# Optimization experiments

Hardware: AMD Instinct MI355X
Metric: run time of the kernel (lower is better)

The kernel has to match this reference:

```python
import jax, jax.numpy as jnp
import numpy as np

N, E, F, H, C, G = 100000, 1600000, 128, 4, 32, 64
D = H * C  # 128, per-layer node dim
NEG_SLOPE = 0.2
BN_EPS = 1e-5


def setup_inputs() -> dict:
    key = jax.random.key(0)
    ks = jax.random.split(key, 24)
    inp = {
        "x": jax.random.normal(ks[0], (N, F), jnp.float32),
        "edge_index": jax.random.randint(ks[1], (2, E), 0, N, jnp.int64),
        "batch": jnp.sort(jax.random.randint(ks[2], (N,), 0, G, jnp.int64)),
        # GATConv layer 0: in=F, out=C per head
        "w0": jax.random.normal(ks[3], (F, H * C), jnp.float32) * 0.1,
        "att_src0": jax.random.normal(ks[4], (H, C), jnp.float32) * 0.1,
        "att_dst0": jax.random.normal(ks[5], (H, C), jnp.float32) * 0.1,
        "bias0": jax.random.normal(ks[6], (H * C,), jnp.float32) * 0.1,
        # GATConv layer 1: in=D, out=C per head
        "w1": jax.random.normal(ks[7], (D, H * C), jnp.float32) * 0.1,
        "att_src1": jax.random.normal(ks[8], (H, C), jnp.float32) * 0.1,
        "att_dst1": jax.random.normal(ks[9], (H, C), jnp.float32) * 0.1,
        "bias1": jax.random.normal(ks[10], (H * C,), jnp.float32) * 0.1,
        # BatchNorm (eval mode: running stats)
        "bn_g0": jax.random.normal(ks[11], (D,), jnp.float32) * 0.1 + 1.0,
        "bn_b0": jax.random.normal(ks[12], (D,), jnp.float32) * 0.1,
        "bn_m0": jax.random.normal(ks[13], (D,), jnp.float32) * 0.1,
        "bn_v0": jax.random.uniform(ks[14], (D,), jnp.float32) + 0.5,
        "bn_g1": jax.random.normal(ks[15], (D,), jnp.float32) * 0.1 + 1.0,
        "bn_b1": jax.random.normal(ks[16], (D,), jnp.float32) * 0.1,
        "bn_m1": jax.random.normal(ks[17], (D,), jnp.float32) * 0.1,
        "bn_v1": jax.random.uniform(ks[18], (D,), jnp.float32) + 0.5,
        # head MLP
        "lin1_w": jax.random.normal(ks[19], (D, D // 2), jnp.float32) * 0.1,
        "lin1_b": jax.random.normal(ks[20], (D // 2,), jnp.float32) * 0.1,
        "lin2_w": jax.random.normal(ks[21], (D // 2, 1), jnp.float32) * 0.1,
        "lin2_b": jax.random.normal(ks[22], (1,), jnp.float32) * 0.1,
    }
    return inp


def gat_conv(x, src, dst, w, att_s, att_d, bias):
    """PyG GATConv (concat=True, add_self_loops already in src/dst), eval mode."""
    n = x.shape[0]
    h = (x @ w).reshape(n, H, C)                       # [N,H,C]
    a_s = jnp.sum(h * att_s, axis=-1)                   # [N,H]
    a_d = jnp.sum(h * att_d, axis=-1)                   # [N,H]
    e = jax.nn.leaky_relu(a_s[src] + a_d[dst], NEG_SLOPE)  # [Etot,H]
    m = jax.ops.segment_max(e, dst, num_segments=n)
    m = jax.lax.stop_gradient(jnp.where(jnp.isfinite(m), m, 0.0))
    ex = jnp.exp(e - m[dst])
    denom = jax.ops.segment_sum(ex, dst, num_segments=n)
    alpha = ex / (denom[dst] + 1e-16)                    # segment softmax over dst
    out = jax.ops.segment_sum(h[src] * alpha[:, :, None], dst, num_segments=n)
    return out.reshape(n, H * C) + bias


def bn_eval(x, g, b, m, v):
    return (x - m) * jax.lax.rsqrt(v + BN_EPS) * g + b


def reference(x, edge_index, batch,
              w0, att_src0, att_dst0, bias0,
              w1, att_src1, att_dst1, bias1,
              bn_g0, bn_b0, bn_m0, bn_v0,
              bn_g1, bn_b1, bn_m1, bn_v1,
              lin1_w, lin1_b, lin2_w, lin2_b):
    n = x.shape[0]
    loops = jnp.arange(n, dtype=edge_index.dtype)
    src = jnp.concatenate([edge_index[0], loops])
    dst = jnp.concatenate([edge_index[1], loops])

    h = gat_conv(x, src, dst, w0, att_src0, att_dst0, bias0)
    h = jax.nn.relu(bn_eval(h, bn_g0, bn_b0, bn_m0, bn_v0))
    h = gat_conv(h, src, dst, w1, att_src1, att_dst1, bias1)
    h = jax.nn.relu(bn_eval(h, bn_g1, bn_b1, bn_m1, bn_v1))

    # global mean pool over graphs
    summed = jax.ops.segment_sum(h, batch, num_segments=G)           # [G,D]
    counts = jax.ops.segment_sum(jnp.ones((n,), h.dtype), batch, num_segments=G)
    pooled = summed / jnp.maximum(counts, 1.0)[:, None]

    z = jax.nn.relu(pooled @ lin1_w + lin1_b)
    return z @ lin2_w + lin2_b                                        # [G,1]
```

## Files before the change

### kernel.cpp

```cpp
#include <hip/hip_runtime.h>

#define GG 64
#define STRIDE 10240
#define NBINMAX 256

typedef __attribute__((ext_vector_type(8))) short short8;
typedef __attribute__((ext_vector_type(4))) float f32x4;


__device__ inline unsigned short bf16rne(float f) {
  unsigned int x = __float_as_uint(f);
  unsigned int r = (x + 0x7FFFu + ((x >> 16) & 1u)) >> 16;
  return (unsigned short)r;
}
__device__ inline unsigned int pack2(float a, float b) {
  return (unsigned int)bf16rne(a) | ((unsigned int)bf16rne(b) << 16);
}
__device__ inline float blo(unsigned int v) { return __uint_as_float(v << 16); }
__device__ inline float bhi(unsigned int v) { return __uint_as_float(v & 0xFFFF0000u); }


__global__ __launch_bounds__(256) void part_p1(const int* __restrict__ ei,
                                               int* __restrict__ gcur,
                                               unsigned int* __restrict__ pairs,
                                               int E, int N) {
  __shared__ int hist[NBINMAX];
  __shared__ int gbase[NBINMAX];
  __shared__ int lcur[NBINMAX];
  int t = threadIdx.x;
  int tot = E + N;
  int base = blockIdx.x * 4096;
  hist[t] = 0;
  __syncthreads();
  int sarr[16], darr[16];
  #pragma unroll
  for (int k = 0; k < 16; ++k) {
    int i = base + k * 256 + t;
    if (i < tot) {
      int s, d;
      if (i < E) { s = ei[i]; d = ei[E + i]; } else { s = i - E; d = s; }
      sarr[k] = s; darr[k] = d;
      atomicAdd(&hist[d >> 9], 1);
    } else darr[k] = -1;
  }
  __syncthreads();
  int c = hist[t];
  gbase[t] = (c > 0) ? atomicAdd(&gcur[t], c) : 0;
  lcur[t] = 0;
  __syncthreads();
  #pragma unroll
  for (int k = 0; k < 16; ++k) {
    int d = darr[k];
    if (d >= 0) {
      int b = d >> 9;
      int p = gbase[b] + atomicAdd(&lcur[b], 1);
      pairs[p] = ((unsigned int)(d & 511) << 17) | (unsigned int)sarr[k];
    }
  }
}


__global__ __launch_bounds__(256) void part_p2(const unsigned int* __restrict__ pairs,
                                               const int* __restrict__ gcur,
                                               int* __restrict__ ssrc,
                                               int* __restrict__ offsets,
                                               int* __restrict__ counts, int N) {
  __shared__ int ncnt[512], ncur[512], excl_s[512];
  __shared__ int wsum[4];
  int b = blockIdx.x;
  int t = threadIdx.x;
  int pb = b * STRIDE;
  int cnt = gcur[b] - pb;
  ncnt[t] = 0; ncnt[t + 256] = 0;
  __syncthreads();
  for (int e = t; e < cnt; e += 256) {
    unsigned int v = pairs[pb + e];
    atomicAdd(&ncnt[v >> 17], 1);
  }
  __syncthreads();
  int c0 = ncnt[2 * t], c1 = ncnt[2 * t + 1];
  int ps = c0 + c1;
  int lane = t & 63, w = t >> 6;
  int x = ps;
  #pragma unroll
  for (int s = 1; s < 64; s <<= 1) { int y = __shfl_up(x, s); if (lane >= s) x += y; }
  if (lane == 63) wsum[w] = x;
  __syncthreads();
  int woff = 0;
  for (int i = 0; i < w; ++i) woff += wsum[i];
  int ep = woff + x - ps;
  excl_s[2 * t]     = ep;
  excl_s[2 * t + 1] = ep + c0;
  __syncthreads();
  int binstart = b << 9;
  for (int i = t; i < 512; i += 256) {
    ncur[i] = excl_s[i];
    int node = binstart + i;
    if (node < N) { offsets[node] = pb + excl_s[i]; counts[node] = ncnt[i]; }
  }
  __syncthreads();
  for (int e = t; e < cnt; e += 256) {
    unsigned int v = pairs[pb + e];
    int dl = v >> 17;
    int p = atomicAdd(&ncur[dl], 1);
    ssrc[pb + p] = (int)(v & 0x1FFFF);
  }
}


__global__ __launch_bounds__(256) void gbounds(const int* __restrict__ batch,
                                               int* __restrict__ gstart, int N) {
  int i = blockIdx.x * 256 + threadIdx.x;
  if (i >= N) return;
  int g = batch[i];
  if (i == 0 || batch[i - 1] != g) gstart[g] = i;
}

__global__ __launch_bounds__(64) void gfix(const int* __restrict__ gstart,
                                           int* __restrict__ go,
                                           int* __restrict__ ge, int N) {
  int g = threadIdx.x;
  int s = gstart[g];
  int v = (s < 0) ? 0x7FFFFFFF : s;
  int suf = v;
  #pragma unroll
  for (int off = 1; off < 64; off <<= 1) {
    int x = __shfl_down(suf, off);
    if (g + off < 64) suf = min(suf, x);
  }
  int nxt = __shfl_down(suf, 1);
  if (g == 63) nxt = 0x7FFFFFFF;
  int e = nxt == 0x7FFFFFFF ? N : nxt;
  if (s < 0) { go[g] = e; ge[g] = e; }
  else       { go[g] = s; ge[g] = e; }
}


__global__ __launch_bounds__(256) void wprep(const float* __restrict__ w0,
                                             const float* __restrict__ w1,
                                             unsigned short* __restrict__ wt,
                                             int* __restrict__ gcur) {
  if (blockIdx.x == 0) gcur[threadIdx.x] = threadIdx.x * STRIDE;
  int idx = blockIdx.x * 256 + threadIdx.x;
  int layer = idx >> 14;
  int e = idx & 16383;
  int k = e >> 7, n = e & 127;
  float v = (layer ? w1 : w0)[e];
  unsigned short hi = bf16rne(v);
  float hif = __uint_as_float((unsigned int)hi << 16);
  unsigned short lo = bf16rne(v - hif);
  unsigned short* basep = wt + layer * 32768;
  basep[n * 128 + k] = hi;
  basep[16384 + n * 128 + k] = lo;
}


template <int BF16IN>
__global__ __launch_bounds__(512) void gemm_mfma(
    const void* __restrict__ in_, const unsigned short* __restrict__ wtL,
    const float* __restrict__ att_s, const float* __restrict__ att_d,
    unsigned int* __restrict__ h16, float* __restrict__ a_s,
    float* __restrict__ a_d, int N) {
  __shared__ unsigned short xh[128][40];
  __shared__ unsigned short xl[BF16IN ? 1 : 128][40];
  int t = threadIdx.x;
  int base = blockIdx.x * 128;
  int lane = t & 63, w = t >> 6;
  int l15 = lane & 15, lg = lane >> 4;
  int hd = w & 3;
  int n0 = hd * 32;
  int rh = w >> 2;

  f32x4 zero4 = {0.f, 0.f, 0.f, 0.f};
  f32x4 acc[4][2];
  #pragma unroll
  for (int rt = 0; rt < 4; ++rt) { acc[rt][0] = zero4; acc[rt][1] = zero4; }

  int sr = t >> 2;
  int sc = (t & 3) * 8;
  int gr = base + sr;
  int rc = gr < N ? gr : (N - 1);
  const float* xpf = (const float*)in_ + (size_t)rc * 128 + sc;
  const unsigned int* xpb = (const unsigned int*)in_ + (size_t)rc * 64 + (sc >> 1);

  const unsigned short* wh0 = &wtL[(size_t)(n0 + l15) * 128];
  const unsigned short* wh1 = &wtL[(size_t)(n0 + 16 + l15) * 128];

  float4 u0, u1;
  uint4 p0;
  if constexpr (!BF16IN) {
    u0 = *(const float4*)(xpf + 0);
    u1 = *(const float4*)(xpf + 4);
  } else {
    p0 = *(const uint4*)(xpb + 0);
  }
  short8 cbh0 = *(const short8*)(wh0 + lg * 8);
  short8 cbh1 = *(const short8*)(wh1 + lg * 8);
  short8 cbl0 = *(const short8*)(wh0 + 16384 + lg * 8);
  short8 cbl1 = *(const short8*)(wh1 + 16384 + lg * 8);

  #pragma unroll
  for (int kt = 0; kt < 4; ++kt) {
    if (kt) __syncthreads();
    if constexpr (!BF16IN) {
      unsigned int b0 = __float_as_uint(u0.x), b1 = __float_as_uint(u0.y);
      unsigned int b2 = __float_as_uint(u0.z), b3 = __float_as_uint(u0.w);
      unsigned int b4 = __float_as_uint(u1.x), b5 = __float_as_uint(u1.y);
      unsigned int b6 = __float_as_uint(u1.z), b7 = __float_as_uint(u1.w);
      *(unsigned int*)&xh[sr][sc + 0] = __builtin_amdgcn_perm(b1, b0, 0x07060302u);
      *(unsigned int*)&xh[sr][sc + 2] = __builtin_amdgcn_perm(b3, b2, 0x07060302u);
      *(unsigned int*)&xh[sr][sc + 4] = __builtin_amdgcn_perm(b5, b4, 0x07060302u);
      *(unsigned int*)&xh[sr][sc + 6] = __builtin_amdgcn_perm(b7, b6, 0x07060302u);
      float r0 = u0.x - __uint_as_float(b0 & 0xFFFF0000u);
      float r1 = u0.y - __uint_as_float(b1 & 0xFFFF0000u);
      float r2 = u0.z - __uint_as_float(b2 & 0xFFFF0000u);
      float r3 = u0.w - __uint_as_float(b3 & 0xFFFF0000u);
      float r4 = u1.x - __uint_as_float(b4 & 0xFFFF0000u);
      float r5 = u1.y - __uint_as_float(b5 & 0xFFFF0000u);
      float r6 = u1.z - __uint_as_float(b6 & 0xFFFF0000u);
      float r7 = u1.w - __uint_as_float(b7 & 0xFFFF0000u);
      *(unsigned int*)&xl[sr][sc + 0] =
          __builtin_amdgcn_perm(__float_as_uint(r1), __float_as_uint(r0), 0x07060302u);
      *(unsigned int*)&xl[sr][sc + 2] =
          __builtin_amdgcn_perm(__float_as_uint(r3), __float_as_uint(r2), 0x07060302u);
      *(unsigned int*)&xl[sr][sc + 4] =
          __builtin_amdgcn_perm(__float_as_uint(r5), __float_as_uint(r4), 0x07060302u);
      *(unsigned int*)&xl[sr][sc + 6] =
          __builtin_amdgcn_perm(__float_as_uint(r7), __float_as_uint(r6), 0x07060302u);
    } else {
      *(uint4*)&xh[sr][sc] = p0;
    }
    __syncthreads();
    float4 v0 = u0, v1 = u1;
    uint4 q0 = p0;
    short8 nbh0 = cbh0, nbh1 = cbh1, nbl0 = cbl0, nbl1 = cbl1;
    if (kt < 3) {
      int k1 = (kt + 1) * 32;
      if constexpr (!BF16IN) {
        v0 = *(const float4*)(xpf + k1);
        v1 = *(const float4*)(xpf + k1 + 4);
      } else {
        q0 = *(const uint4*)(xpb + (k1 >> 1));
      }
      nbh0 = *(const short8*)(wh0 + k1 + lg * 8);
      nbh1 = *(const short8*)(wh1 + k1 + lg * 8);
      nbl0 = *(const short8*)(wh0 + 16384 + k1 + lg * 8);
      nbl1 = *(const short8*)(wh1 + 16384 + k1 + lg * 8);
    }
    #pragma unroll
    for (int rt = 0; rt < 4; ++rt) {
      int row = rh * 64 + rt * 16 + l15;
      short8 fah = *(const short8*)&xh[row][lg * 8];
      acc[rt][0] = __builtin_amdgcn_mfma_f32_16x16x32_bf16(fah, cbh0, acc[rt][0], 0, 0, 0);
      acc[rt][1] = __builtin_amdgcn_mfma_f32_16x16x32_bf16(fah, cbh1, acc[rt][1], 0, 0, 0);
      if constexpr (!BF16IN) {
        short8 fal = *(const short8*)&xl[row][lg * 8];
        acc[rt][0] = __builtin_amdgcn_mfma_f32_16x16x32_bf16(fal, cbh0, acc[rt][0], 0, 0, 0);
        acc[rt][1] = __builtin_amdgcn_mfma_f32_16x16x32_bf16(fal, cbh1, acc[rt][1], 0, 0, 0);
      }
      acc[rt][0] = __builtin_amdgcn_mfma_f32_16x16x32_bf16(fah, cbl0, acc[rt][0], 0, 0, 0);
      acc[rt][1] = __builtin_amdgcn_mfma_f32_16x16x32_bf16(fah, cbl1, acc[rt][1], 0, 0, 0);
    }
    u0 = v0; u1 = v1; p0 = q0;
    cbh0 = nbh0; cbh1 = nbh1; cbl0 = nbl0; cbl1 = nbl1;
  }

  int headg = hd;
  float as0 = att_s[n0 + l15], as1 = att_s[n0 + 16 + l15];
  float ad0 = att_d[n0 + l15], ad1 = att_d[n0 + 16 + l15];
  #pragma unroll
  for (int rt = 0; rt < 4; ++rt) {
    float ps[4], pd[4];
    #pragma unroll
    for (int q = 0; q < 4; ++q) {
      float c0v = acc[rt][0][q], c1v = acc[rt][1][q];
      float pp0 = __shfl_xor(c0v, 1), pp1 = __shfl_xor(c1v, 1);
      int row = base + rh * 64 + rt * 16 + lg * 4 + q;
      if (!(l15 & 1) && row < N) {
        h16[(size_t)row * 64 + (n0 + l15) / 2]      = pack2(c0v, pp0);
        h16[(size_t)row * 64 + (n0 + 16 + l15) / 2] = pack2(c1v, pp1);
      }
      ps[q] = c0v * as0 + c1v * as1;
      pd[q] = c0v * ad0 + c1v * ad1;
    }
    #pragma unroll
    for (int m = 1; m <= 8; m <<= 1) {
      #pragma unroll
      for (int q = 0; q < 4; ++q) { ps[q] += __shfl_xor(ps[q], m); pd[q] += __shfl_xor(pd[q], m); }
    }
    if (l15 == 0) {
      #pragma unroll
      for (int q = 0; q < 4; ++q) {
        int row = base + rh * 64 + rt * 16 + lg * 4 + q;
        if (row < N) { a_s[row * 4 + headg] = ps[q]; a_d[row * 4 + headg] = pd[q]; }
      }
    }
  }
}


#define ACCP(EX, V0, V1)                                                       \
  { float2 ex2 = make_float2(EX, EX);                                          \
    acc2[0] += ex2 * make_float2(blo(V0.x), bhi(V0.x));                        \
    acc2[1] += ex2 * make_float2(blo(V0.y), bhi(V0.y));                        \
    acc2[2] += ex2 * make_float2(blo(V0.z), bhi(V0.z));                        \
    acc2[3] += ex2 * make_float2(blo(V0.w), bhi(V0.w));                        \
    acc2[4] += ex2 * make_float2(blo(V1.x), bhi(V1.x));                        \
    acc2[5] += ex2 * make_float2(blo(V1.y), bhi(V1.y));                        \
    acc2[6] += ex2 * make_float2(blo(V1.z), bhi(V1.z));                        \
    acc2[7] += ex2 * make_float2(blo(V1.w), bhi(V1.w)); }

__global__ __launch_bounds__(256) void gat_aggregate(
    const unsigned int* __restrict__ h16, const float* __restrict__ a_s, const float* __restrict__ a_d,
    const int* __restrict__ offsets, const int* __restrict__ counts, const int* __restrict__ ssrc,
    const float* __restrict__ bias,
    const float* __restrict__ bn_g, const float* __restrict__ bn_b,
    const float* __restrict__ bn_m, const float* __restrict__ bn_v,
    unsigned int* __restrict__ y16, int N) {
  __shared__ float part[4][8][132];
  int wv = threadIdx.x >> 6;
  int lane = threadIdx.x & 63;
  int wid = blockIdx.x * 4 + wv;
  if (wid >= N) return;
  int off = offsets[wid], cnt = counts[wid];
  int eg = lane >> 3;
  int j  = lane & 7;
  int hh = j >> 1;
  float ad = a_d[wid * 4 + hh];

  float2 acc2[8] = {};
  float den = 0.f;

  int sA = ssrc[off + (eg < cnt ? eg : 0)];
  int iB0 = eg + 8;
  int sB = ssrc[off + (iB0 < cnt ? iB0 : 0)];
  float asA = a_s[sA * 4 + hh];
  float asB = a_s[sB * 4 + hh];

  for (int i = eg; i < cnt; i += 16) {
    const uint4* hpA = (const uint4*)(h16 + (size_t)sA * 64 + j * 8);
    uint4 va0 = hpA[0], va1 = hpA[1];
    const uint4* hpB = (const uint4*)(h16 + (size_t)sB * 64 + j * 8);
    uint4 vb0 = hpB[0], vb1 = hpB[1];
    int in0 = i + 16, in1 = i + 24;
    int snA = ssrc[off + (in0 < cnt ? in0 : 0)];
    int snB = ssrc[off + (in1 < cnt ? in1 : 0)];
    float anA = a_s[snA * 4 + hh];
    float anB = a_s[snB * 4 + hh];
    float eA = asA + ad; eA = eA > 0.f ? eA : 0.2f * eA;
    float exA = __expf(eA);
    float eB = asB + ad; eB = eB > 0.f ? eB : 0.2f * eB;
    float exB = ((i + 8) < cnt) ? __expf(eB) : 0.f;
    den += exA + exB;
    ACCP(exA, va0, va1)
    ACCP(exB, vb0, vb1)
    sA = snA; sB = snB; asA = anA; asB = anB;
  }

  den += __shfl_xor(den, 8);
  den += __shfl_xor(den, 16);
  den += __shfl_xor(den, 32);
  den = __shfl(den, (lane >> 4) * 2);

  float* pw = &part[wv][eg][j * 16];
  *(float4*)(pw + 0)  = make_float4(acc2[0].x, acc2[0].y, acc2[1].x, acc2[1].y);
  *(float4*)(pw + 4)  = make_float4(acc2[2].x, acc2[2].y, acc2[3].x, acc2[3].y);
  *(float4*)(pw + 8)  = make_float4(acc2[4].x, acc2[4].y, acc2[5].x, acc2[5].y);
  *(float4*)(pw + 12) = make_float4(acc2[6].x, acc2[6].y, acc2[7].x, acc2[7].y);
  asm volatile("s_waitcnt lgkmcnt(0)" ::: "memory");

  int d = lane * 2;
  float r0 = 0.f, r1 = 0.f;
  #pragma unroll
  for (int g = 0; g < 8; ++g) {
    float2 v = *(const float2*)(&part[wv][g][d]);
    r0 += v.x; r1 += v.y;
  }

  float inv = 1.f / (den + 1e-16f);
  float2 bi = *(const float2*)(&bias[d]);
  float2 g2 = *(const float2*)(&bn_g[d]);
  float2 b2 = *(const float2*)(&bn_b[d]);
  float2 m2 = *(const float2*)(&bn_m[d]);
  float2 v2 = *(const float2*)(&bn_v[d]);
  float o0 = r0 * inv + bi.x;
  float o1 = r1 * inv + bi.y;
  o0 = fmaxf((o0 - m2.x) * (g2.x * rsqrtf(v2.x + 1e-5f)) + b2.x, 0.f);
  o1 = fmaxf((o1 - m2.y) * (g2.y * rsqrtf(v2.y + 1e-5f)) + b2.y, 0.f);
  y16[(size_t)wid * 64 + lane] = pack2(o0, o1);
}


#define POOLP 8

__global__ __launch_bounds__(256) void pool_kernel(const unsigned int* __restrict__ y16,
                                                   const int* __restrict__ go,
                                                   const int* __restrict__ ge,
                                                   float* __restrict__ pooled) {
  int g = blockIdx.x / POOLP, p = blockIdx.x % POOLP;
  int s = go[g], e = ge[g];
  int len = e - s;
  int q0 = s + (len * p) / POOLP, q1 = s + (len * (p + 1)) / POOLP;
  int t = threadIdx.x;
  int d = t & 127, half = t >> 7;
  int du = d >> 1, dodd = d & 1;
  float acc = 0.f;
  for (int i = q0 + half; i < q1; i += 2) {
    unsigned int v = y16[(size_t)i * 64 + du];
    acc += dodd ? bhi(v) : blo(v);
  }
  __shared__ float red[256];
  red[t] = acc;
  __syncthreads();
  if (half == 0) atomicAdd(&pooled[g * 128 + d], red[d] + red[d + 128]);
}

__global__ __launch_bounds__(64) void mlp_kernel(const float* __restrict__ pooled,
                                                 const int* __restrict__ go,
                                                 const int* __restrict__ ge,
                                                 const float* __restrict__ w1,
                                                 const float* __restrict__ b1,
                                                 const float* __restrict__ w2,
                                                 const float* __restrict__ b2,
                                                 float* __restrict__ out) {
  int g = blockIdx.x, j = threadIdx.x;
  int cnt = ge[g] - go[g];
  float inv = 1.f / (float)(cnt > 1 ? cnt : 1);
  float z = b1[j];
  for (int k = 0; k < 128; ++k) z += pooled[g * 128 + k] * inv * w1[k * 64 + j];
  z = fmaxf(z, 0.f);
  float v = z * w2[j];
  #pragma unroll
  for (int m = 1; m < 64; m <<= 1) v += __shfl_xor(v, m);
  if (j == 0) out[g] = v + b2[0];
}


extern "C" void kernel_launch(void* const* d_in, const int* in_sizes, int n_in,
                              void* d_out, int out_size, void* d_ws, size_t ws_size,
                              hipStream_t stream) {
  const float* x     = (const float*)d_in[0];
  const int*   ei    = (const int*)d_in[1];
  const int*   batch = (const int*)d_in[2];
  const float* w0    = (const float*)d_in[3];
  const float* atts0 = (const float*)d_in[4];
  const float* attd0 = (const float*)d_in[5];
  const float* bias0 = (const float*)d_in[6];
  const float* w1    = (const float*)d_in[7];
  const float* atts1 = (const float*)d_in[8];
  const float* attd1 = (const float*)d_in[9];
  const float* bias1 = (const float*)d_in[10];
  const float* bng0  = (const float*)d_in[11];
  const float* bnb0  = (const float*)d_in[12];
  const float* bnm0  = (const float*)d_in[13];
  const float* bnv0  = (const float*)d_in[14];
  const float* bng1  = (const float*)d_in[15];
  const float* bnb1  = (const float*)d_in[16];
  const float* bnm1  = (const float*)d_in[17];
  const float* bnv1  = (const float*)d_in[18];
  const float* l1w   = (const float*)d_in[19];
  const float* l1b   = (const float*)d_in[20];
  const float* l2w   = (const float*)d_in[21];
  const float* l2b   = (const float*)d_in[22];

  int N = in_sizes[2];
  int E = in_sizes[1] / 2;
  int tot = E + N;
  int NBIN = (N + 511) / 512;

  char* p = (char*)d_ws;
  unsigned int* h16 = (unsigned int*)p; p += (size_t)N * 64 * 4;
  unsigned int* y16 = (unsigned int*)p; p += (size_t)N * 64 * 4;
  float* a_s    = (float*)p; p += (size_t)N * 4 * 4;
  float* a_d    = (float*)p; p += (size_t)N * 4 * 4;
  int* counts   = (int*)p;   p += (size_t)N * 4;
  int* offsets  = (int*)p;   p += (size_t)N * 4;
  int* ssrc     = (int*)p;   p += (size_t)NBINMAX * STRIDE * 4;
  int* gcur     = (int*)p;   p += NBINMAX * 4;
  int* gstart   = (int*)p;   p += 64 * 4;
  int* go       = (int*)p;   p += 64 * 4;
  int* ge       = (int*)p;   p += 64 * 4;
  float* pooled = (float*)p; p += 64 * 128 * 4;
  unsigned short* wt = (unsigned short*)p; p += 2 * 32768 * 2;
  unsigned int* pairs = y16;

  hipMemsetAsync(gstart, 0xFF, 64 * 4, stream);
  hipMemsetAsync(pooled, 0, 64 * 128 * 4, stream);

  int bN = (N + 255) / 256;
  int bW = (N + 3) / 4;
  int bG = (N + 127) / 128;

  wprep<<<128, 256, 0, stream>>>(w0, w1, wt, gcur);
  part_p1<<<(tot + 4095) / 4096, 256, 0, stream>>>(ei, gcur, pairs, E, N);
  part_p2<<<NBIN, 256, 0, stream>>>(pairs, gcur, ssrc, offsets, counts, N);
  gbounds<<<bN, 256, 0, stream>>>(batch, gstart, N);
  gfix<<<1, 64, 0, stream>>>(gstart, go, ge, N);

  gemm_mfma<0><<<bG, 512, 0, stream>>>(x, wt, atts0, attd0, h16, a_s, a_d, N);
  gat_aggregate<<<bW, 256, 0, stream>>>(h16, a_s, a_d, offsets, counts, ssrc,
                                        bias0, bng0, bnb0, bnm0, bnv0, y16, N);
  gemm_mfma<1><<<bG, 512, 0, stream>>>(y16, wt + 32768, atts1, attd1, h16, a_s, a_d, N);
  gat_aggregate<<<bW, 256, 0, stream>>>(h16, a_s, a_d, offsets, counts, ssrc,
                                        bias1, bng1, bnb1, bnm1, bnv1, y16, N);
  pool_kernel<<<GG * POOLP, 256, 0, stream>>>(y16, go, ge, pooled);
  mlp_kernel<<<GG, 64, 0, stream>>>(pooled, go, ge, l1w, l1b, l2w, l2b, (float*)d_out);
}
```

Before: 312.8 us.

## Fuse first GEMM, edge partition and graph-bounds into combined launches

Merges the layer-0 MFMA GEMM, the edge-partition pass 1 and the batch-boundary detection into one heterogeneous kernel that dispatches on block index. It also merges partition pass 2 with the graph-range fixup into a second kernel. The goal is fewer launches and letting independent preprocessing run alongside the GEMM. In exchange, partition-1 blocks now run with 512 threads, and the whole fused kernel is sized for the GEMM's shared memory and register budget, which may reduce occupancy.

```diff
diff --git a/kernel.cpp b/kernel.cpp
--- a/kernel.cpp
+++ b/kernel.cpp
@@ -18,122 +18,6 @@
 }
 __device__ inline float blo(unsigned int v) { return __uint_as_float(v << 16); }
 __device__ inline float bhi(unsigned int v) { return __uint_as_float(v & 0xFFFF0000u); }
-
-
-__global__ __launch_bounds__(256) void part_p1(const int* __restrict__ ei,
-                                               int* __restrict__ gcur,
-                                               unsigned int* __restrict__ pairs,
-                                               int E, int N) {
-  __shared__ int hist[NBINMAX];
-  __shared__ int gbase[NBINMAX];
-  __shared__ int lcur[NBINMAX];
-  int t = threadIdx.x;
-  int tot = E + N;
-  int base = blockIdx.x * 4096;
-  hist[t] = 0;
-  __syncthreads();
-  int sarr[16], darr[16];
-  #pragma unroll
-  for (int k = 0; k < 16; ++k) {
-    int i = base + k * 256 + t;
-    if (i < tot) {
-      int s, d;
-      if (i < E) { s = ei[i]; d = ei[E + i]; } else { s = i - E; d = s; }
-      sarr[k] = s; darr[k] = d;
-      atomicAdd(&hist[d >> 9], 1);
-    } else darr[k] = -1;
-  }
-  __syncthreads();
-  int c = hist[t];
-  gbase[t] = (c > 0) ? atomicAdd(&gcur[t], c) : 0;
-  lcur[t] = 0;
-  __syncthreads();
-  #pragma unroll
-  for (int k = 0; k < 16; ++k) {
-    int d = darr[k];
-    if (d >= 0) {
-      int b = d >> 9;
-      int p = gbase[b] + atomicAdd(&lcur[b], 1);
-      pairs[p] = ((unsigned int)(d & 511) << 17) | (unsigned int)sarr[k];
-    }
-  }
-}
-
-
-__global__ __launch_bounds__(256) void part_p2(const unsigned int* __restrict__ pairs,
-                                               const int* __restrict__ gcur,
-                                               int* __restrict__ ssrc,
-                                               int* __restrict__ offsets,
-                                               int* __restrict__ counts, int N) {
-  __shared__ int ncnt[512], ncur[512], excl_s[512];
-  __shared__ int wsum[4];
-  int b = blockIdx.x;
-  int t = threadIdx.x;
-  int pb = b * STRIDE;
-  int cnt = gcur[b] - pb;
-  ncnt[t] = 0; ncnt[t + 256] = 0;
-  __syncthreads();
-  for (int e = t; e < cnt; e += 256) {
-    unsigned int v = pairs[pb + e];
-    atomicAdd(&ncnt[v >> 17], 1);
-  }
-  __syncthreads();
-  int c0 = ncnt[2 * t], c1 = ncnt[2 * t + 1];
-  int ps = c0 + c1;
-  int lane = t & 63, w = t >> 6;
-  int x = ps;
-  #pragma unroll
-  for (int s = 1; s < 64; s <<= 1) { int y = __shfl_up(x, s); if (lane >= s) x += y; }
-  if (lane == 63) wsum[w] = x;
-  __syncthreads();
-  int woff = 0;
-  for (int i = 0; i < w; ++i) woff += wsum[i];
-  int ep = woff + x - ps;
-  excl_s[2 * t]     = ep;
-  excl_s[2 * t + 1] = ep + c0;
-  __syncthreads();
-  int binstart = b << 9;
-  for (int i = t; i < 512; i += 256) {
-    ncur[i] = excl_s[i];
-    int node = binstart + i;
-    if (node < N) { offsets[node] = pb + excl_s[i]; counts[node] = ncnt[i]; }
-  }
-  __syncthreads();
-  for (int e = t; e < cnt; e += 256) {
-    unsigned int v = pairs[pb + e];
-    int dl = v >> 17;
-    int p = atomicAdd(&ncur[dl], 1);
-    ssrc[pb + p] = (int)(v & 0x1FFFF);
-  }
-}
-
-
-__global__ __launch_bounds__(256) void gbounds(const int* __restrict__ batch,
-                                               int* __restrict__ gstart, int N) {
-  int i = blockIdx.x * 256 + threadIdx.x;
-  if (i >= N) return;
-  int g = batch[i];
-  if (i == 0 || batch[i - 1] != g) gstart[g] = i;
-}
-
-__global__ __launch_bounds__(64) void gfix(const int* __restrict__ gstart,
-                                           int* __restrict__ go,
-                                           int* __restrict__ ge, int N) {
-  int g = threadIdx.x;
-  int s = gstart[g];
-  int v = (s < 0) ? 0x7FFFFFFF : s;
-  int suf = v;
-  #pragma unroll
-  for (int off = 1; off < 64; off <<= 1) {
-    int x = __shfl_down(suf, off);
-    if (g + off < 64) suf = min(suf, x);
-  }
-  int nxt = __shfl_down(suf, 1);
-  if (g == 63) nxt = 0x7FFFFFFF;
-  int e = nxt == 0x7FFFFFFF ? N : nxt;
-  if (s < 0) { go[g] = e; ge[g] = e; }
-  else       { go[g] = s; ge[g] = e; }
-}
 
 
 __global__ __launch_bounds__(256) void wprep(const float* __restrict__ w0,
@@ -155,14 +39,248 @@
 }
 
 
-template <int BF16IN>
-__global__ __launch_bounds__(512) void gemm_mfma(
-    const void* __restrict__ in_, const unsigned short* __restrict__ wtL,
+__global__ __launch_bounds__(512) void mega1(
+    const float* __restrict__ in, const unsigned short* __restrict__ wtL,
+    const float* __restrict__ att_s, const float* __restrict__ att_d,
+    unsigned int* __restrict__ h16, float* __restrict__ a_s, float* __restrict__ a_d,
+    const int* __restrict__ ei, int* __restrict__ gcur, unsigned int* __restrict__ pairs,
+    const int* __restrict__ batch, int* __restrict__ gstart,
+    int N, int E, int bG, int P1B) {
+  __shared__ unsigned short xh[128][40], xl[128][40];
+  __shared__ int hist[NBINMAX], gbase[NBINMAX], lcur[NBINMAX];
+  int bid = blockIdx.x;
+  int t = threadIdx.x;
+
+  if (bid < bG) {
+    int base = bid * 128;
+    int lane = t & 63, w = t >> 6;
+    int l15 = lane & 15, lg = lane >> 4;
+    int hd = w & 3;
+    int n0 = hd * 32;
+    int rh = w >> 2;
+
+    f32x4 zero4 = {0.f, 0.f, 0.f, 0.f};
+    f32x4 acc[4][2];
+    #pragma unroll
+    for (int rt = 0; rt < 4; ++rt) { acc[rt][0] = zero4; acc[rt][1] = zero4; }
+
+    int sr = t >> 2;
+    int sc = (t & 3) * 8;
+    int gr = base + sr;
+    int rc = gr < N ? gr : (N - 1);
+    const float* xpf = in + (size_t)rc * 128 + sc;
+
+    const unsigned short* wh0 = &wtL[(size_t)(n0 + l15) * 128];
+    const unsigned short* wh1 = &wtL[(size_t)(n0 + 16 + l15) * 128];
+
+    float4 u0 = *(const float4*)(xpf + 0);
+    float4 u1 = *(const float4*)(xpf + 4);
+    short8 cbh0 = *(const short8*)(wh0 + lg * 8);
+    short8 cbh1 = *(const short8*)(wh1 + lg * 8);
+    short8 cbl0 = *(const short8*)(wh0 + 16384 + lg * 8);
+    short8 cbl1 = *(const short8*)(wh1 + 16384 + lg * 8);
+
+    #pragma unroll
+    for (int kt = 0; kt < 4; ++kt) {
+      if (kt) __syncthreads();
+      {
+        unsigned int b0 = __float_as_uint(u0.x), b1 = __float_as_uint(u0.y);
+        unsigned int b2 = __float_as_uint(u0.z), b3 = __float_as_uint(u0.w);
+        unsigned int b4 = __float_as_uint(u1.x), b5 = __float_as_uint(u1.y);
+        unsigned int b6 = __float_as_uint(u1.z), b7 = __float_as_uint(u1.w);
+        *(unsigned int*)&xh[sr][sc + 0] = __builtin_amdgcn_perm(b1, b0, 0x07060302u);
+        *(unsigned int*)&xh[sr][sc + 2] = __builtin_amdgcn_perm(b3, b2, 0x07060302u);
+        *(unsigned int*)&xh[sr][sc + 4] = __builtin_amdgcn_perm(b5, b4, 0x07060302u);
+        *(unsigned int*)&xh[sr][sc + 6] = __builtin_amdgcn_perm(b7, b6, 0x07060302u);
+        float r0 = u0.x - __uint_as_float(b0 & 0xFFFF0000u);
+        float r1 = u0.y - __uint_as_float(b1 & 0xFFFF0000u);
+        float r2 = u0.z - __uint_as_float(b2 & 0xFFFF0000u);
+        float r3 = u0.w - __uint_as_float(b3 & 0xFFFF0000u);
+        float r4 = u1.x - __uint_as_float(b4 & 0xFFFF0000u);
+        float r5 = u1.y - __uint_as_float(b5 & 0xFFFF0000u);
+        float r6 = u1.z - __uint_as_float(b6 & 0xFFFF0000u);
+        float r7 = u1.w - __uint_as_float(b7 & 0xFFFF0000u);
+        *(unsigned int*)&xl[sr][sc + 0] =
+            __builtin_amdgcn_perm(__float_as_uint(r1), __float_as_uint(r0), 0x07060302u);
+        *(unsigned int*)&xl[sr][sc + 2] =
+            __builtin_amdgcn_perm(__float_as_uint(r3), __float_as_uint(r2), 0x07060302u);
+        *(unsigned int*)&xl[sr][sc + 4] =
+            __builtin_amdgcn_perm(__float_as_uint(r5), __float_as_uint(r4), 0x07060302u);
+        *(unsigned int*)&xl[sr][sc + 6] =
+            __builtin_amdgcn_perm(__float_as_uint(r7), __float_as_uint(r6), 0x07060302u);
+      }
+      __syncthreads();
+      float4 v0 = u0, v1 = u1;
+      short8 nbh0 = cbh0, nbh1 = cbh1, nbl0 = cbl0, nbl1 = cbl1;
+      if (kt < 3) {
+        int k1 = (kt + 1) * 32;
+        v0 = *(const float4*)(xpf + k1);
+        v1 = *(const float4*)(xpf + k1 + 4);
+        nbh0 = *(const short8*)(wh0 + k1 + lg * 8);
+        nbh1 = *(const short8*)(wh1 + k1 + lg * 8);
+        nbl0 = *(const short8*)(wh0 + 16384 + k1 + lg * 8);
+        nbl1 = *(const short8*)(wh1 + 16384 + k1 + lg * 8);
+      }
+      #pragma unroll
+      for (int rt = 0; rt < 4; ++rt) {
+        int row = rh * 64 + rt * 16 + l15;
+        short8 fah = *(const short8*)&xh[row][lg * 8];
+        short8 fal = *(const short8*)&xl[row][lg * 8];
+        acc[rt][0] = __builtin_amdgcn_mfma_f32_16x16x32_bf16(fah, cbh0, acc[rt][0], 0, 0, 0);
+        acc[rt][1] = __builtin_amdgcn_mfma_f32_16x16x32_bf16(fah, cbh1, acc[rt][1], 0, 0, 0);
+        acc[rt][0] = __builtin_amdgcn_mfma_f32_16x16x32_bf16(fal, cbh0, acc[rt][0], 0, 0, 0);
+        acc[rt][1] = __builtin_amdgcn_mfma_f32_16x16x32_bf16(fal, cbh1, acc[rt][1], 0, 0, 0);
+        acc[rt][0] = __builtin_amdgcn_mfma_f32_16x16x32_bf16(fah, cbl0, acc[rt][0], 0, 0, 0);
+        acc[rt][1] = __builtin_amdgcn_mfma_f32_16x16x32_bf16(fah, cbl1, acc[rt][1], 0, 0, 0);
+      }
+      u0 = v0; u1 = v1;
+      cbh0 = nbh0; cbh1 = nbh1; cbl0 = nbl0; cbl1 = nbl1;
+    }
+
+    int headg = hd;
+    float as0 = att_s[n0 + l15], as1 = att_s[n0 + 16 + l15];
+    float ad0 = att_d[n0 + l15], ad1 = att_d[n0 + 16 + l15];
+    #pragma unroll
+    for (int rt = 0; rt < 4; ++rt) {
+      float ps[4], pd[4];
+      #pragma unroll
+      for (int q = 0; q < 4; ++q) {
+        float c0v = acc[rt][0][q], c1v = acc[rt][1][q];
+        float pp0 = __shfl_xor(c0v, 1), pp1 = __shfl_xor(c1v, 1);
+        int row = base + rh * 64 + rt * 16 + lg * 4 + q;
+        if (!(l15 & 1) && row < N) {
+          h16[(size_t)row * 64 + (n0 + l15) / 2]      = pack2(c0v, pp0);
+          h16[(size_t)row * 64 + (n0 + 16 + l15) / 2] = pack2(c1v, pp1);
+        }
+        ps[q] = c0v * as0 + c1v * as1;
+        pd[q] = c0v * ad0 + c1v * ad1;
+      }
+      #pragma unroll
+      for (int m = 1; m <= 8; m <<= 1) {
+        #pragma unroll
+        for (int q = 0; q < 4; ++q) { ps[q] += __shfl_xor(ps[q], m); pd[q] += __shfl_xor(pd[q], m); }
+      }
+      if (l15 == 0) {
+        #pragma unroll
+        for (int q = 0; q < 4; ++q) {
+          int row = base + rh * 64 + rt * 16 + lg * 4 + q;
+          if (row < N) { a_s[row * 4 + headg] = ps[q]; a_d[row * 4 + headg] = pd[q]; }
+        }
+      }
+    }
+  } else if (bid < bG + P1B) {
+    int tot = E + N;
+    int base = (bid - bG) * 4096;
+    if (t < NBINMAX) hist[t] = 0;
+    __syncthreads();
+    int sarr[8], darr[8];
+    #pragma unroll
+    for (int k = 0; k < 8; ++k) {
+      int i = base + k * 512 + t;
+      if (i < tot) {
+        int s, d;
+        if (i < E) { s = ei[i]; d = ei[E + i]; } else { s = i - E; d = s; }
+        sarr[k] = s; darr[k] = d;
+        atomicAdd(&hist[d >> 9], 1);
+      } else darr[k] = -1;
+    }
+    __syncthreads();
+    if (t < NBINMAX) {
+      int c = hist[t];
+      gbase[t] = (c > 0) ? atomicAdd(&gcur[t], c) : 0;
+      lcur[t] = 0;
+    }
+    __syncthreads();
+    #pragma unroll
+    for (int k = 0; k < 8; ++k) {
+      int d = darr[k];
+      if (d >= 0) {
+        int b = d >> 9;
+        int p = gbase[b] + atomicAdd(&lcur[b], 1);
+        pairs[p] = ((unsigned int)(d & 511) << 17) | (unsigned int)sarr[k];
+      }
+    }
+  } else {
+    int i = (bid - bG - P1B) * 512 + t;
+    if (i < N) {
+      int g = batch[i];
+      if (i == 0 || batch[i - 1] != g) gstart[g] = i;
+    }
+  }
+}
+
+
+__global__ __launch_bounds__(256) void mega2(
+    const unsigned int* __restrict__ pairs, const int* __restrict__ gcur,
+    int* __restrict__ ssrc, int* __restrict__ offsets, int* __restrict__ counts,
+    const int* __restrict__ gstart, int* __restrict__ go, int* __restrict__ ge,
+    int N, int NBIN) {
+  __shared__ int ncnt[512], ncur[512], excl_s[512];
+  __shared__ int wsum[4];
+  int b = blockIdx.x;
+  int t = threadIdx.x;
+  if (b < NBIN) {
+    int pb = b * STRIDE;
+    int cnt = gcur[b] - pb;
+    ncnt[t] = 0; ncnt[t + 256] = 0;
+    __syncthreads();
+    for (int e = t; e < cnt; e += 256) {
+      unsigned int v = pairs[pb + e];
+      atomicAdd(&ncnt[v >> 17], 1);
+    }
+    __syncthreads();
+    int c0 = ncnt[2 * t], c1 = ncnt[2 * t + 1];
+    int ps = c0 + c1;
+    int lane = t & 63, w = t >> 6;
+    int x = ps;
+    #pragma unroll
+    for (int s = 1; s < 64; s <<= 1) { int y = __shfl_up(x, s); if (lane >= s) x += y; }
+    if (lane == 63) wsum[w] = x;
+    __syncthreads();
+    int woff = 0;
+    for (int i = 0; i < w; ++i) woff += wsum[i];
+    int ep = woff + x - ps;
+    excl_s[2 * t]     = ep;
+    excl_s[2 * t + 1] = ep + c0;
+    __syncthreads();
+    int binstart = b << 9;
+    for (int i = t; i < 512; i += 256) {
+      ncur[i] = excl_s[i];
+      int node = binstart + i;
+      if (node < N) { offsets[node] = pb + excl_s[i]; counts[node] = ncnt[i]; }
+    }
+    __syncthreads();
+    for (int e = t; e < cnt; e += 256) {
+      unsigned int v = pairs[pb + e];
+      int dl = v >> 17;
+      int p = atomicAdd(&ncur[dl], 1);
+      ssrc[pb + p] = (int)(v & 0x1FFFF);
+    }
+  } else if (t < 64) {
+    int g = t;
+    int s = gstart[g];
+    int v = (s < 0) ? 0x7FFFFFFF : s;
+    int suf = v;
+    #pragma unroll
+    for (int off = 1; off < 64; off <<= 1) {
+      int x = __shfl_down(suf, off);
+      if (g + off < 64) suf = min(suf, x);
+    }
+    int nxt = __shfl_down(suf, 1);
+    if (g == 63) nxt = 0x7FFFFFFF;
+    int e = nxt == 0x7FFFFFFF ? N : nxt;
+    if (s < 0) { go[g] = e; ge[g] = e; }
+    else       { go[g] = s; ge[g] = e; }
+  }
+}
+
+
+__global__ __launch_bounds__(512) void gemm_bf16(
+    const unsigned int* __restrict__ in, const unsigned short* __restrict__ wtL,
     const float* __restrict__ att_s, const float* __restrict__ att_d,
     unsigned int* __restrict__ h16, float* __restrict__ a_s,
     float* __restrict__ a_d, int N) {
   __shared__ unsigned short xh[128][40];
-  __shared__ unsigned short xl[BF16IN ? 1 : 128][40];
   int t = threadIdx.x;
   int base = blockIdx.x * 128;
   int lane = t & 63, w = t >> 6;
@@ -180,20 +298,12 @@
   int sc = (t & 3) * 8;
   int gr = base + sr;
   int rc = gr < N ? gr : (N - 1);
-  const float* xpf = (const float*)in_ + (size_t)rc * 128 + sc;
-  const unsigned int* xpb = (const unsigned int*)in_ + (size_t)rc * 64 + (sc >> 1);
+  const unsigned int* xpb = in + (size_t)rc * 64 + (sc >> 1);
 
   const unsigned short* wh0 = &wtL[(size_t)(n0 + l15) * 128];
   const unsigned short* wh1 = &wtL[(size_t)(n0 + 16 + l15) * 128];
 
-  float4 u0, u1;
-  uint4 p0;
-  if constexpr (!BF16IN) {
-    u0 = *(const float4*)(xpf + 0);
-    u1 = *(const float4*)(xpf + 4);
-  } else {
-    p0 = *(const uint4*)(xpb + 0);
-  }
+  uint4 p0 = *(const uint4*)(xpb + 0);
   short8 cbh0 = *(const short8*)(wh0 + lg * 8);
   short8 cbh1 = *(const short8*)(wh1 + lg * 8);
   short8 cbl0 = *(const short8*)(wh0 + 16384 + lg * 8);
@@ -202,46 +312,13 @@
   #pragma unroll
   for (int kt = 0; kt < 4; ++kt) {
     if (kt) __syncthreads();
-    if constexpr (!BF16IN) {
-      unsigned int b0 = __float_as_uint(u0.x), b1 = __float_as_uint(u0.y);
-      unsigned int b2 = __float_as_uint(u0.z), b3 = __float_as_uint(u0.w);
-      unsigned int b4 = __float_as_uint(u1.x), b5 = __float_as_uint(u1.y);
-      unsigned int b6 = __float_as_uint(u1.z), b7 = __float_as_uint(u1.w);
-      *(unsigned int*)&xh[sr][sc + 0] = __builtin_amdgcn_perm(b1, b0, 0x07060302u);
-      *(unsigned int*)&xh[sr][sc + 2] = __builtin_amdgcn_perm(b3, b2, 0x07060302u);
-      *(unsigned int*)&xh[sr][sc + 4] = __builtin_amdgcn_perm(b5, b4, 0x07060302u);
-      *(unsigned int*)&xh[sr][sc + 6] = __builtin_amdgcn_perm(b7, b6, 0x07060302u);
-      float r0 = u0.x - __uint_as_float(b0 & 0xFFFF0000u);
-      float r1 = u0.y - __uint_as_float(b1 & 0xFFFF0000u);
-      float r2 = u0.z - __uint_as_float(b2 & 0xFFFF0000u);
-      float r3 = u0.w - __uint_as_float(b3 & 0xFFFF0000u);
-      float r4 = u1.x - __uint_as_float(b4 & 0xFFFF0000u);
-      float r5 = u1.y - __uint_as_float(b5 & 0xFFFF0000u);
-      float r6 = u1.z - __uint_as_float(b6 & 0xFFFF0000u);
-      float r7 = u1.w - __uint_as_float(b7 & 0xFFFF0000u);
-      *(unsigned int*)&xl[sr][sc + 0] =
-          __builtin_amdgcn_perm(__float_as_uint(r1), __float_as_uint(r0), 0x07060302u);
-      *(unsigned int*)&xl[sr][sc + 2] =
-          __builtin_amdgcn_perm(__float_as_uint(r3), __float_as_uint(r2), 0x07060302u);
-      *(unsigned int*)&xl[sr][sc + 4] =
-          __builtin_amdgcn_perm(__float_as_uint(r5), __float_as_uint(r4), 0x07060302u);
-      *(unsigned int*)&xl[sr][sc + 6] =
-          __builtin_amdgcn_perm(__float_as_uint(r7), __float_as_uint(r6), 0x07060302u);
-    } else {
-      *(uint4*)&xh[sr][sc] = p0;
-    }
-    __syncthreads();
-    float4 v0 = u0, v1 = u1;
+    *(uint4*)&xh[sr][sc] = p0;
+    __syncthreads();
     uint4 q0 = p0;
     short8 nbh0 = cbh0, nbh1 = cbh1, nbl0 = cbl0, nbl1 = cbl1;
     if (kt < 3) {
       int k1 = (kt + 1) * 32;
-      if constexpr (!BF16IN) {
-        v0 = *(const float4*)(xpf + k1);
-        v1 = *(const float4*)(xpf + k1 + 4);
-      } else {
-        q0 = *(const uint4*)(xpb + (k1 >> 1));
-      }
+      q0 = *(const uint4*)(xpb + (k1 >> 1));
       nbh0 = *(const short8*)(wh0 + k1 + lg * 8);
       nbh1 = *(const short8*)(wh1 + k1 + lg * 8);
       nbl0 = *(const short8*)(wh0 + 16384 + k1 + lg * 8);
@@ -253,15 +330,10 @@
       short8 fah = *(const short8*)&xh[row][lg * 8];
       acc[rt][0] = __builtin_amdgcn_mfma_f32_16x16x32_bf16(fah, cbh0, acc[rt][0], 0, 0, 0);
       acc[rt][1] = __builtin_amdgcn_mfma_f32_16x16x32_bf16(fah, cbh1, acc[rt][1], 0, 0, 0);
-      if constexpr (!BF16IN) {
-        short8 fal = *(const short8*)&xl[row][lg * 8];
-        acc[rt][0] = __builtin_amdgcn_mfma_f32_16x16x32_bf16(fal, cbh0, acc[rt][0], 0, 0, 0);
-        acc[rt][1] = __builtin_amdgcn_mfma_f32_16x16x32_bf16(fal, cbh1, acc[rt][1], 0, 0, 0);
-      }
       acc[rt][0] = __builtin_amdgcn_mfma_f32_16x16x32_bf16(fah, cbl0, acc[rt][0], 0, 0, 0);
       acc[rt][1] = __builtin_amdgcn_mfma_f32_16x16x32_bf16(fah, cbl1, acc[rt][1], 0, 0, 0);
     }
-    u0 = v0; u1 = v1; p0 = q0;
+    p0 = q0;
     cbh0 = nbh0; cbh1 = nbh1; cbl0 = nbl0; cbl1 = nbl1;
   }
 
@@ -487,20 +559,20 @@
   hipMemsetAsync(gstart, 0xFF, 64 * 4, stream);
   hipMemsetAsync(pooled, 0, 64 * 128 * 4, stream);
 
-  int bN = (N + 255) / 256;
   int bW = (N + 3) / 4;
   int bG = (N + 127) / 128;
+  int P1B = (tot + 4095) / 4096;
+  int BNB = (N + 511) / 512;
 
   wprep<<<128, 256, 0, stream>>>(w0, w1, wt, gcur);
-  part_p1<<<(tot + 4095) / 4096, 256, 0, stream>>>(ei, gcur, pairs, E, N);
-  part_p2<<<NBIN, 256, 0, stream>>>(pairs, gcur, ssrc, offsets, counts, N);
-  gbounds<<<bN, 256, 0, stream>>>(batch, gstart, N);
-  gfix<<<1, 64, 0, stream>>>(gstart, go, ge, N);
-
-  gemm_mfma<0><<<bG, 512, 0, stream>>>(x, wt, atts0, attd0, h16, a_s, a_d, N);
+  mega1<<<bG + P1B + BNB, 512, 0, stream>>>(x, wt, atts0, attd0, h16, a_s, a_d,
+                                            ei, gcur, pairs, batch, gstart,
+                                            N, E, bG, P1B);
+  mega2<<<NBIN + 1, 256, 0, stream>>>(pairs, gcur, ssrc, offsets, counts,
+                                      gstart, go, ge, N, NBIN);
   gat_aggregate<<<bW, 256, 0, stream>>>(h16, a_s, a_d, offsets, counts, ssrc,
                                         bias0, bng0, bnb0, bnm0, bnv0, y16, N);
-  gemm_mfma<1><<<bG, 512, 0, stream>>>(y16, wt + 32768, atts1, attd1, h16, a_s, a_d, N);
+  gemm_bf16<<<bG, 512, 0, stream>>>(y16, wt + 32768, atts1, attd1, h16, a_s, a_d, N);
   gat_aggregate<<<bW, 256, 0, stream>>>(h16, a_s, a_d, offsets, counts, ssrc,
                                         bias1, bng1, bnb1, bnm1, bnv1, y16, N);
   pool_kernel<<<GG * POOLP, 256, 0, stream>>>(y16, go, ge, pooled);
```

After: 293.4 us. 6.2% less time.
